# Kernel tuning notes

Hardware: AMD Instinct MI355X
Metric: run time of the kernel (lower is better)

## Reference

```python
import jax, jax.numpy as jnp
import numpy as np

DM, EXP, N, K, FRAC = 1024, 2, 16, 4, 16
D = DM * EXP            # working_dim = 2048
DTR = D // FRAC         # delta low-rank dim = 128
EPS = 1e-6


def setup_inputs() -> dict:
    key = jax.random.key(0)
    ks = jax.random.split(key, 12)
    s = lambda fan: 1.0 / np.sqrt(fan)
    x = jax.random.normal(ks[0], (2, 1024, DM), jnp.float32)
    rms_w = jnp.ones((DM,), jnp.float32)
    in_W = jax.random.normal(ks[1], (DM, 2 * D), jnp.float32) * s(DM)
    in_b = jax.random.normal(ks[2], (2 * D,), jnp.float32) * s(DM)
    conv_w = jax.random.normal(ks[3], (D, K), jnp.float32) * s(K)
    conv_b = jax.random.normal(ks[4], (D,), jnp.float32) * s(K)
    # A = arange(1..N) repeated over channels, stored as log
    A_log = jnp.log(jnp.tile(jnp.arange(1, N + 1, dtype=jnp.float32), (D, 1)))
    dbc_W = jax.random.normal(ks[5], (D, DTR + 2 * N), jnp.float32) * s(D)
    dbc_b = jax.random.normal(ks[6], (DTR + 2 * N,), jnp.float32) * s(D)
    dup_W = jax.random.normal(ks[7], (DTR, D), jnp.float32) * s(DTR)
    dup_b = jax.random.normal(ks[8], (D,), jnp.float32) * s(DTR)
    out_W = jax.random.normal(ks[9], (D, DM), jnp.float32) * s(D)
    out_b = jax.random.normal(ks[10], (DM,), jnp.float32) * s(D)
    return dict(x=x, rms_w=rms_w, in_W=in_W, in_b=in_b, conv_w=conv_w,
                conv_b=conv_b, A_log=A_log, dbc_W=dbc_W, dbc_b=dbc_b,
                dup_W=dup_W, dup_b=dup_b, out_W=out_W, out_b=out_b)


def _mamba_block(x, rms_w, in_W, in_b, conv_w, conv_b, A_log,
                 dbc_W, dbc_b, dup_W, dup_b, out_W, out_b):
    residual = x
    # RMSNorm
    h = x * jax.lax.rsqrt(jnp.mean(x * x, axis=-1, keepdims=True) + EPS) * rms_w
    # in projection -> (x1, g)
    proj = h @ in_W + in_b
    x1, g = proj[..., :D], proj[..., D:]
    # depthwise causal conv (torch pads K-1 both sides then keeps first T == left-pad K-1)
    xt = jnp.transpose(x1, (0, 2, 1))                      # [B, D, T]
    xc = jax.lax.conv_general_dilated(
        xt, conv_w[:, None, :], window_strides=(1,), padding=[(K - 1, 0)],
        feature_group_count=D, dimension_numbers=("NCH", "OIH", "NCH"))
    xc = xc + conv_b[:, None]
    x1 = jax.nn.silu(jnp.transpose(xc, (0, 2, 1)))         # [B, T, D]
    # selective SSM
    A = -jnp.exp(A_log)                                    # [D, N]
    dbc = x1 @ dbc_W + dbc_b
    delta, Bm, Cm = dbc[..., :DTR], dbc[..., DTR:DTR + N], dbc[..., DTR + N:]
    delta = jax.nn.softplus(delta @ dup_W + dup_b)         # [B, T, D]
    A_disc = jnp.exp(delta[..., None] * A)                 # [B, T, D, N]
    B_x = delta[..., None] * Bm[:, :, None, :] * x1[..., None]  # [B, T, D, N]
    # time-major sequential scan: h_t = A_t * h_{t-1} + Bx_t
    Ad_t = jnp.transpose(A_disc, (1, 0, 2, 3))
    Bx_t = jnp.transpose(B_x, (1, 0, 2, 3))

    def step(hc, inp):
        a, b = inp
        hc = a * hc + b
        return hc, hc

    h0 = jnp.zeros((x.shape[0], D, N), x1.dtype)
    _, hs = jax.lax.scan(step, h0, (Ad_t, Bx_t))           # [T, B, D, N]
    y = jnp.einsum("tbdn,btn->btd", hs, Cm)                # [B, T, D]
    # gate and out projection
    y = jax.nn.silu(g) * y
    out = y @ out_W + out_b
    return out + residual


def reference(x, rms_w, in_W, in_b, conv_w, conv_b, A_log,
              dbc_W, dbc_b, dup_W, dup_b, out_W, out_b):
    return _mamba_block(x, rms_w, in_W, in_b, conv_w, conv_b, A_log,
                        dbc_W, dbc_b, dup_W, dup_b, out_W, out_b)
```

## Files before the change

### kernel.cpp

```cpp
#include <hip/hip_runtime.h>
#include <math.h>

typedef unsigned short us;
typedef __attribute__((ext_vector_type(8))) short frag8;
typedef __attribute__((ext_vector_type(8))) unsigned short u8v;
typedef __attribute__((ext_vector_type(4))) float f4;
typedef __attribute__((ext_vector_type(2))) float f2;

#define B_   2
#define T_   1024
#define DM_  1024
#define D_   2048
#define N_   16
#define DTR_ 128
#define NDBC 160
#define ROWS (B_*T_)
#define EPS_ 1e-6f
#define NCH  32
#define CLEN (T_/NCH)
#define KSPL 8
#define OSPL 4
#define L2E  1.44269504f

__device__ __forceinline__ float us2f(us s){
    return __uint_as_float(((unsigned int)s) << 16);
}
__device__ __forceinline__ us f2us(float f){
    unsigned int u = __float_as_uint(f);
    return (us)((u + 0x7FFF + ((u >> 16) & 1)) >> 16);
}
__device__ __forceinline__ float exp2i(float x){
    float r; asm("v_exp_f32 %0, %1" : "=v"(r) : "v"(x)); return r;
}
__device__ __forceinline__ float rcpi(float x){
    return __builtin_amdgcn_rcpf(x);
}

__device__ __forceinline__ void async16(const void* g, void* l){
    __builtin_amdgcn_global_load_lds(
        (const __attribute__((address_space(1))) void*)g,
        (__attribute__((address_space(3)))       void*)l, 16, 0, 0);
}

template<int CTRL>
__device__ __forceinline__ float dpp_add(float x){
    int t = __builtin_amdgcn_update_dpp(0, __float_as_int(x), CTRL, 0xF, 0xF, true);
    return x + __int_as_float(t);
}
__device__ __forceinline__ float sum4_quad(float x){
    x = dpp_add<0xB1>(x);
    x = dpp_add<0x4E>(x);
    return x;
}

__global__ __launch_bounds__(256) void prep_weights(
    const float* __restrict__ in_W,  const float* __restrict__ out_W,
    const float* __restrict__ dbc_W, const float* __restrict__ dup_W,
    us* __restrict__ inWt, us* __restrict__ outWt,
    us* __restrict__ dbcWt, us* __restrict__ dupWt,
    const float* __restrict__ x, const float* __restrict__ rms_w,
    us* __restrict__ hbf)
{
    int bid = blockIdx.x;
    int tx = threadIdx.x, ty = threadIdx.y;
    if (bid >= 6720) {
        const int row = bid - 6720;
        const int tid = ty * 32 + tx;
        const float* xr = x + (size_t)row * DM_;
        float vals[4], ss = 0.f;
#pragma unroll
        for (int i = 0; i < 4; ++i) { vals[i] = xr[tid + i*256]; ss += vals[i]*vals[i]; }
#pragma unroll
        for (int off = 32; off >= 1; off >>= 1) ss += __shfl_xor(ss, off, 64);
        __shared__ float red[4];
        if ((tid & 63) == 0) red[tid >> 6] = ss;
        __syncthreads();
        float scale = rsqrtf((red[0]+red[1]+red[2]+red[3]) / (float)DM_ + EPS_);
#pragma unroll
        for (int i = 0; i < 4; ++i)
            hbf[(size_t)row * DM_ + tid + i*256] = f2us(vals[i] * scale * rms_w[tid + i*256]);
        return;
    }
    __shared__ us tile[32][33];
    const float* src; us* dst; int C, R, TX, rel;
    if (bid < 4096)      { src = in_W;  dst = inWt;  R = 1024; C = 4096; TX = 128; rel = bid; }
    else if (bid < 6144) { src = out_W; dst = outWt; R = 2048; C = 1024; TX = 32;  rel = bid - 4096; }
    else if (bid < 6464) { src = dbc_W; dst = dbcWt; R = 2048; C = 160;  TX = 5;   rel = bid - 6144; }
    else                 { src = dup_W; dst = dupWt; R = 128;  C = 2048; TX = 64;  rel = bid - 6464; }
    int c0 = (rel % TX) * 32, r0 = (rel / TX) * 32;
    for (int i = ty; i < 32; i += 8)
        tile[i][tx] = f2us(src[(size_t)(r0 + i) * C + c0 + tx]);
    __syncthreads();
    for (int i = ty; i < 32; i += 8)
        dst[(size_t)(c0 + i) * R + r0 + tx] = tile[tx][i];
}

__global__ __launch_bounds__(256) void transpose_us(const us* __restrict__ in,
                                                    us* __restrict__ out, int R, int C)
{
    __shared__ us tile[32][33];
    int c0 = blockIdx.x * 32, r0 = blockIdx.y * 32;
    int tx = threadIdx.x, ty = threadIdx.y;
    for (int i = ty; i < 32; i += 8)
        tile[i][tx] = in[(size_t)(r0 + i) * C + c0 + tx];
    __syncthreads();
    for (int i = ty; i < 32; i += 8)
        out[(size_t)(c0 + i) * R + r0 + tx] = tile[tx][i];
}

template<int EPI, bool RB>
__global__ __launch_bounds__(256) void mgemm(
    const us*    __restrict__ A,
    const us*    __restrict__ Bt,
    const float* __restrict__ bias,
    float*       __restrict__ Cf,
    us*          __restrict__ Caux,
    const float* __restrict__ resid,
    float*       __restrict__ bct,
    int M, int N, int K, int ld)
{
    __shared__ us As[128*64];
    __shared__ us Bs[128*64];
    const int tid = threadIdx.x;
    const int bm = blockIdx.y * 128;
    const int bn = blockIdx.x * 128;
    const int w = tid >> 6, lane = tid & 63;
    const int wr = w >> 1, wc = w & 1;
    const int m16 = lane & 15, quad = lane >> 4;

    const us* Ak = A;
    const us* Bk = Bt;
    if constexpr (EPI == 5) {
        const size_t koff = (size_t)blockIdx.z * K;
        Ak += koff; Bk += koff;
        Cf += (size_t)blockIdx.z * (size_t)M * N;
    }

    f4 acc[4][4];
#pragma unroll
    for (int i = 0; i < 4; ++i)
#pragma unroll
        for (int j = 0; j < 4; ++j)
            acc[i][j] = (f4){0.f, 0.f, 0.f, 0.f};

    for (int k0 = 0; k0 < K; k0 += 64) {
        __syncthreads();
#pragma unroll
        for (int q = 0; q < 4; ++q) {
            int cb = (w*4 + q)*64 + lane;
            int row = cb >> 3, c8 = (cb & 7)*8;
            async16(Ak + (size_t)(bm + row) * ld + k0 + c8, &As[cb*8]);
            async16(Bk + (size_t)(bn + row) * ld + k0 + c8, &Bs[cb*8]);
        }
        __syncthreads();
#pragma unroll
        for (int ks = 0; ks < 64; ks += 32) {
            frag8 af[4], bfr[4];
#pragma unroll
            for (int i = 0; i < 4; ++i)
                af[i] = *(const frag8*)&As[(wr*64 + i*16 + m16)*64 + ks + quad*8];
#pragma unroll
            for (int j = 0; j < 4; ++j)
                bfr[j] = *(const frag8*)&Bs[(wc*64 + j*16 + m16)*64 + ks + quad*8];
#pragma unroll
            for (int i = 0; i < 4; ++i)
#pragma unroll
                for (int j = 0; j < 4; ++j)
                    acc[i][j] = __builtin_amdgcn_mfma_f32_16x16x32_bf16(af[i], bfr[j], acc[i][j], 0, 0, 0);
        }
    }

#pragma unroll
    for (int i = 0; i < 4; ++i) {
#pragma unroll
        for (int j = 0; j < 4; ++j) {
            int col = bn + wc*64 + j*16 + m16;
            if (col >= N) continue;
            float bvc = (RB || EPI == 5) ? 0.f : bias[col];
#pragma unroll
            for (int r = 0; r < 4; ++r) {
                int row = bm + wr*64 + i*16 + quad*4 + r;
                float v = acc[i][j][r] + (EPI == 5 ? 0.f : (RB ? bias[row] : bvc));
                if constexpr (EPI == 1) {
                    v = fmaxf(v, 0.f) + __logf(1.f + __expf(-fabsf(v)));
                    Cf[(size_t)row * N + col] = v;
                } else if constexpr (EPI == 2) {
                    v += resid[(size_t)row * N + col];
                    Cf[(size_t)row * N + col] = v;
                } else if constexpr (EPI == 3) {
                    if (col < DTR_) Caux[(size_t)row * DTR_ + col] = f2us(v);
                    else            bct [(size_t)row * 32 + (col - DTR_)] = v;
                } else if constexpr (EPI == 4) {
                    if (col < D_) Cf  [(size_t)row * D_ + col]        = v;
                    else          Caux[(size_t)row * D_ + (col - D_)] = f2us(v);
                } else {
                    Cf[(size_t)row * N + col] = v;
                }
            }
        }
    }
}

__global__ __launch_bounds__(256) void dbc_reduce(
    const float* __restrict__ part,
    const float* __restrict__ bias,
    us*    __restrict__ dtrb,
    float* __restrict__ bct)
{
    int idx = blockIdx.x * 256 + threadIdx.x;
    int row = idx / NDBC, col = idx - row * NDBC;
    float v = bias[col];
#pragma unroll
    for (int z = 0; z < KSPL; ++z)
        v += part[(size_t)z * ROWS * NDBC + idx];
    if (col < DTR_) dtrb[(size_t)row * DTR_ + col] = f2us(v);
    else            bct [(size_t)row * 32 + (col - DTR_)] = v;
}

__global__ __launch_bounds__(256) void out_reduce(
    const float* __restrict__ part,
    const float* __restrict__ bias,
    const float* __restrict__ resid,
    float* __restrict__ out)
{
    int idx = (blockIdx.x * 256 + threadIdx.x) * 4;
    int col = idx & (DM_ - 1);
    f4 v = *(const f4*)&bias[col];
    v += *(const f4*)&resid[idx];
#pragma unroll
    for (int z = 0; z < OSPL; ++z)
        v += *(const f4*)&part[(size_t)z * ROWS * DM_ + idx];
    *(f4*)&out[idx] = v;
}

__global__ __launch_bounds__(256) void conv_silu_kernel(
    const float* __restrict__ x1pre,
    const us*    __restrict__ g_rm,
    const float* __restrict__ cw,
    const float* __restrict__ cb,
    us*          __restrict__ x1cb,
    us*          __restrict__ x1tb,
    us*          __restrict__ g_t)
{
    __shared__ us tileX[32][33];
    __shared__ us tileG[32][33];
    const int tx = threadIdx.x, ty = threadIdx.y;
    const int d0 = blockIdx.x * 32, r0 = blockIdx.y * 32;
    const int d = d0 + tx;
    const float w0 = cw[d*4+0], w1 = cw[d*4+1], w2 = cw[d*4+2], w3 = cw[d*4+3];
    const float bias = cb[d];
    for (int i = ty; i < 32; i += 8) {
        int row = r0 + i;
        int t = row & (T_ - 1);
        const float* base = x1pre + (size_t)row * D_ + d;
        float acc = bias;
        acc = fmaf(w3, base[0], acc);
        if (t >= 1) acc = fmaf(w2, base[-D_],   acc);
        if (t >= 2) acc = fmaf(w1, base[-2*D_], acc);
        if (t >= 3) acc = fmaf(w0, base[-3*D_], acc);
        float sg = rcpi(1.f + exp2i(-acc * L2E));
        us uv = f2us(acc * sg);
        x1cb[(size_t)row * D_ + d] = uv;
        tileX[i][tx] = uv;
        tileG[i][tx] = g_rm[(size_t)row * D_ + d];
    }
    __syncthreads();
    for (int i = ty; i < 32; i += 8) {
        x1tb[(size_t)(d0 + i) * ROWS + r0 + tx] = tileX[tx][i];
        g_t [(size_t)(d0 + i) * ROWS + r0 + tx] = tileG[tx][i];
    }
}

__global__ __launch_bounds__(128, 4) void scan_block_kernel(
    const float* __restrict__ delta_t,
    const us*    __restrict__ x1tb,
    const float* __restrict__ bct,
    const float* __restrict__ A_log,
    const us*    __restrict__ g_t,
    us*          __restrict__ y_t)
{
    __shared__ float ysA[T_ + NCH];
    __shared__ float ysB[T_ + NCH];
    __shared__ f4 PSl[2][NCH][9];

    const int tid = threadIdx.x;
    const int pr = blockIdx.x & (D_/2 - 1);
    const int b  = blockIdx.x >> 10;
    const int d0 = pr * 2;
    const int ng = tid & 3;
    const int c  = tid >> 2;
    const size_t rb  = (size_t)b * T_;
    const size_t cb0 = (size_t)d0 * ROWS + rb;
    const int t0 = c * CLEN;

    f4 al0 = *(const f4*)&A_log[d0 * N_ + ng * 4];
    f4 al1 = *(const f4*)&A_log[(d0 + 1) * N_ + ng * 4];
    const f2 aA01 = (f2){-__expf(al0[0])*L2E, -__expf(al0[1])*L2E};
    const f2 aA23 = (f2){-__expf(al0[2])*L2E, -__expf(al0[3])*L2E};
    const f2 aB01 = (f2){-__expf(al1[0])*L2E, -__expf(al1[1])*L2E};
    const f2 aB23 = (f2){-__expf(al1[2])*L2E, -__expf(al1[3])*L2E};

    const float* __restrict__ dpA = delta_t + cb0 + t0;
    const float* __restrict__ dpB = dpA + ROWS;
    const us*    __restrict__ xpA = x1tb + cb0 + t0;
    const us*    __restrict__ xpB = xpA + ROWS;
    const float* __restrict__ bp = bct + (size_t)(rb + t0) * 32 + ng * 4;
    const float* __restrict__ cp = bp + 16;

    float DsA = 0.f, DsB = 0.f;
    f2 SA01={0.f,0.f}, SA23={0.f,0.f};
    f2 SB01={0.f,0.f}, SB23={0.f,0.f};
#pragma unroll
    for (int g = 0; g < 4; ++g) {
        f4 dA0 = *(const f4*)&dpA[g*8], dA1 = *(const f4*)&dpA[g*8 + 4];
        f4 dB0 = *(const f4*)&dpB[g*8], dB1 = *(const f4*)&dpB[g*8 + 4];
        u8v xA = *(const u8v*)&xpA[g*8];
        u8v xB = *(const u8v*)&xpB[g*8];
#pragma unroll
        for (int j = 0; j < 8; ++j) {
            float djA = (j < 4) ? dA0[j] : dA1[j-4];
            float djB = (j < 4) ? dB0[j] : dB1[j-4];
            f4 Bv = *(const f4*)&bp[(size_t)(g*8 + j) * 32];
            float dxA = djA * us2f(xA[j]);
            float dxB = djB * us2f(xB[j]);
            DsA += djA; DsB += djB;
            f2 jA = (f2){djA, djA}, jB = (f2){djB, djB};
            f2 eA01 = jA*aA01, eA23 = jA*aA23;
            f2 eB01 = jB*aB01, eB23 = jB*aB23;
            f2 xA01 = (f2){exp2i(eA01.x), exp2i(eA01.y)};
            f2 xA23 = (f2){exp2i(eA23.x), exp2i(eA23.y)};
            f2 xB01 = (f2){exp2i(eB01.x), exp2i(eB01.y)};
            f2 xB23 = (f2){exp2i(eB23.x), exp2i(eB23.y)};
            SA01 = xA01*SA01 + (f2){dxA*Bv[0], dxA*Bv[1]};
            SA23 = xA23*SA23 + (f2){dxA*Bv[2], dxA*Bv[3]};
            SB01 = xB01*SB01 + (f2){dxB*Bv[0], dxB*Bv[1]};
            SB23 = xB23*SB23 + (f2){dxB*Bv[2], dxB*Bv[3]};
        }
    }
    f2 PA01 = (f2){exp2i(aA01.x*DsA), exp2i(aA01.y*DsA)};
    f2 PA23 = (f2){exp2i(aA23.x*DsA), exp2i(aA23.y*DsA)};
    f2 PB01 = (f2){exp2i(aB01.x*DsB), exp2i(aB01.y*DsB)};
    f2 PB23 = (f2){exp2i(aB23.x*DsB), exp2i(aB23.y*DsB)};
    PSl[0][c][2*ng+0] = (f4){PA01.x,PA01.y,SA01.x,SA01.y};
    PSl[0][c][2*ng+1] = (f4){PA23.x,PA23.y,SA23.x,SA23.y};
    PSl[1][c][2*ng+0] = (f4){PB01.x,PB01.y,SB01.x,SB01.y};
    PSl[1][c][2*ng+1] = (f4){PB23.x,PB23.y,SB23.x,SB23.y};
    __syncthreads();

    f2 hA01={0.f,0.f}, hA23={0.f,0.f}, hB01={0.f,0.f}, hB23={0.f,0.f};
    for (int c2 = 0; c2 < c; ++c2) {
        f4 p0 = PSl[0][c2][2*ng+0], p1 = PSl[0][c2][2*ng+1];
        f4 q0 = PSl[1][c2][2*ng+0], q1 = PSl[1][c2][2*ng+1];
        hA01 = (f2){p0[0],p0[1]}*hA01 + (f2){p0[2],p0[3]};
        hA23 = (f2){p1[0],p1[1]}*hA23 + (f2){p1[2],p1[3]};
        hB01 = (f2){q0[0],q0[1]}*hB01 + (f2){q0[2],q0[3]};
        hB23 = (f2){q1[0],q1[1]}*hB23 + (f2){q1[2],q1[3]};
    }

#pragma unroll
    for (int g = 0; g < 4; ++g) {
        f4 dA0 = *(const f4*)&dpA[g*8], dA1 = *(const f4*)&dpA[g*8 + 4];
        f4 dB0 = *(const f4*)&dpB[g*8], dB1 = *(const f4*)&dpB[g*8 + 4];
        u8v xA = *(const u8v*)&xpA[g*8];
        u8v xB = *(const u8v*)&xpB[g*8];
#pragma unroll
        for (int j = 0; j < 8; ++j) {
            float djA = (j < 4) ? dA0[j] : dA1[j-4];
            float djB = (j < 4) ? dB0[j] : dB1[j-4];
            f4 Bv = *(const f4*)&bp[(size_t)(g*8 + j) * 32];
            f4 Cv = *(const f4*)&cp[(size_t)(g*8 + j) * 32];
            float dxA = djA * us2f(xA[j]);
            float dxB = djB * us2f(xB[j]);
            f2 jA = (f2){djA, djA}, jB = (f2){djB, djB};
            f2 eA01 = jA*aA01, eA23 = jA*aA23;
            f2 eB01 = jB*aB01, eB23 = jB*aB23;
            f2 xA01 = (f2){exp2i(eA01.x), exp2i(eA01.y)};
            f2 xA23 = (f2){exp2i(eA23.x), exp2i(eA23.y)};
            f2 xB01 = (f2){exp2i(eB01.x), exp2i(eB01.y)};
            f2 xB23 = (f2){exp2i(eB23.x), exp2i(eB23.y)};
            hA01 = xA01*hA01 + (f2){dxA*Bv[0], dxA*Bv[1]};
            hA23 = xA23*hA23 + (f2){dxA*Bv[2], dxA*Bv[3]};
            hB01 = xB01*hB01 + (f2){dxB*Bv[0], dxB*Bv[1]};
            hB23 = xB23*hB23 + (f2){dxB*Bv[2], dxB*Bv[3]};
            float sA = (hA01.x*Cv[0] + hA01.y*Cv[1]) + (hA23.x*Cv[2] + hA23.y*Cv[3]);
            float sB = (hB01.x*Cv[0] + hB01.y*Cv[1]) + (hB23.x*Cv[2] + hB23.y*Cv[3]);
            sA = sum4_quad(sA);
            sB = sum4_quad(sB);
            int t = t0 + g*8 + j;
            if (ng == 0) { ysA[t + (t >> 5)] = sA; ysB[t + (t >> 5)] = sB; }
        }
    }
    __syncthreads();

    {
        int i = tid * 8;
        int fi = i + (i >> 5);
        u8v ugA = *(const u8v*)&g_t[cb0 + i];
        u8v ugB = *(const u8v*)&g_t[cb0 + ROWS + i];
        u8v uyA, uyB;
#pragma unroll
        for (int k = 0; k < 8; ++k) {
            float gA = us2f(ugA[k]), gB = us2f(ugB[k]);
            uyA[k] = f2us(ysA[fi + k] * gA * rcpi(1.f + exp2i(-gA * L2E)));
            uyB[k] = f2us(ysB[fi + k] * gB * rcpi(1.f + exp2i(-gB * L2E)));
        }
        *(u8v*)&y_t[cb0 + i] = uyA;
        *(u8v*)&y_t[cb0 + ROWS + i] = uyB;
    }
}

extern "C" void kernel_launch(void* const* d_in, const int* in_sizes, int n_in,
                              void* d_out, int out_size, void* d_ws, size_t ws_size,
                              hipStream_t stream)
{
    const float* x      = (const float*)d_in[0];
    const float* rms_w  = (const float*)d_in[1];
    const float* in_W   = (const float*)d_in[2];
    const float* in_b   = (const float*)d_in[3];
    const float* conv_w = (const float*)d_in[4];
    const float* conv_b = (const float*)d_in[5];
    const float* A_log  = (const float*)d_in[6];
    const float* dbc_W  = (const float*)d_in[7];
    const float* dbc_b  = (const float*)d_in[8];
    const float* dup_W  = (const float*)d_in[9];
    const float* dup_b  = (const float*)d_in[10];
    const float* out_W  = (const float*)d_in[11];
    const float* out_b  = (const float*)d_in[12];
    float* out = (float*)d_out;

    float* ws      = (float*)d_ws;
    float* x1pre   = ws;
    us* g_rm  = (us*)(x1pre + (size_t)ROWS*D_);
    us* g_t   = g_rm  + (size_t)ROWS*D_;
    float* bct     = (float*)(g_t + (size_t)ROWS*D_);
    float* delta_t = bct + (size_t)2*N_*ROWS;
    us* hbf   = (us*)(delta_t + (size_t)ROWS*D_);
    us* x1cb  = hbf   + (size_t)ROWS*DM_;
    us* x1tb  = x1cb  + (size_t)ROWS*D_;
    us* dtrb  = x1tb  + (size_t)ROWS*D_;
    us* inWt  = dtrb  + (size_t)ROWS*DTR_;
    us* dbcWt = inWt  + (size_t)2*D_*DM_;
    us* dupWt = dbcWt + (size_t)NDBC*D_;
    us* outWt = dupWt + (size_t)D_*DTR_;
    float* dbcPart = x1pre;
    us* y_t   = (us*)x1pre;
    us* ybf   = x1cb;
    float* outPart = x1pre;
    dim3 tb(32, 8);
    prep_weights<<<6720 + ROWS, tb, 0, stream>>>(in_W, out_W, dbc_W, dup_W,
                                                 inWt, outWt, dbcWt, dupWt,
                                                 x, rms_w, hbf);
    mgemm<4,false><<<dim3(32, 16), 256, 0, stream>>>(
        hbf, inWt, in_b, x1pre, g_rm, nullptr, nullptr, ROWS, 2*D_, DM_, DM_);
    conv_silu_kernel<<<dim3(D_/32, ROWS/32), tb, 0, stream>>>(
        x1pre, g_rm, conv_w, conv_b, x1cb, x1tb, g_t);
    mgemm<5,false><<<dim3(2, 16, KSPL), 256, 0, stream>>>(
        x1cb, dbcWt, nullptr, dbcPart, nullptr, nullptr, nullptr,
        ROWS, NDBC, D_/KSPL, D_);
    dbc_reduce<<<ROWS*NDBC/256, 256, 0, stream>>>(dbcPart, dbc_b, dtrb, bct);
    mgemm<1,true><<<dim3(16, 16), 256, 0, stream>>>(
        dupWt, dtrb, dup_b, delta_t, nullptr, nullptr, nullptr, D_, ROWS, DTR_, DTR_);
    scan_block_kernel<<<B_*D_/2, 128, 0, stream>>>(delta_t, x1tb, bct, A_log, g_t, y_t);
    transpose_us<<<dim3(ROWS/32, D_/32), tb, 0, stream>>>(y_t, ybf, D_, ROWS);
    mgemm<5,false><<<dim3(8, 16, OSPL), 256, 0, stream>>>(
        ybf, outWt, nullptr, outPart, nullptr, nullptr, nullptr,
        ROWS, DM_, D_/OSPL, D_);
    out_reduce<<<ROWS*DM_/1024, 256, 0, stream>>>(outPart, out_b, x, out);
}
```

Baseline: 244.2 us.

## Fuse y transpose into scan epilogue and swizzle GEMM block order

The scan kernel now writes the gated output straight into the row-major bf16 buffer used by the out projection, packing the two channels as one 32-bit store per timestep. This removes the separate transpose kernel and its round trip through memory. The GEMM kernels also remap block indices with an 8-way swizzle, intended to improve L2 reuse across blocks that run at the same time. The fused stores are strided 4-byte writes (stride D_), so they are poorly coalesced. The swizzle assumes the grid size is divisible by 8.

```diff
diff --git a/kernel.cpp b/kernel.cpp
--- a/kernel.cpp
+++ b/kernel.cpp
@@ -95,19 +95,6 @@
         dst[(size_t)(c0 + i) * R + r0 + tx] = tile[tx][i];
 }
 
-__global__ __launch_bounds__(256) void transpose_us(const us* __restrict__ in,
-                                                    us* __restrict__ out, int R, int C)
-{
-    __shared__ us tile[32][33];
-    int c0 = blockIdx.x * 32, r0 = blockIdx.y * 32;
-    int tx = threadIdx.x, ty = threadIdx.y;
-    for (int i = ty; i < 32; i += 8)
-        tile[i][tx] = in[(size_t)(r0 + i) * C + c0 + tx];
-    __syncthreads();
-    for (int i = ty; i < 32; i += 8)
-        out[(size_t)(c0 + i) * R + r0 + tx] = tile[tx][i];
-}
-
 template<int EPI, bool RB>
 __global__ __launch_bounds__(256) void mgemm(
     const us*    __restrict__ A,
@@ -122,8 +109,12 @@
     __shared__ us As[128*64];
     __shared__ us Bs[128*64];
     const int tid = threadIdx.x;
-    const int bm = blockIdx.y * 128;
-    const int bn = blockIdx.x * 128;
+    const int nx  = gridDim.x;
+    const int lin = blockIdx.y * nx + blockIdx.x;
+    const int cpx = (nx * gridDim.y) >> 3;
+    const int swz = (lin & 7) * cpx + (lin >> 3);
+    const int bm = (swz / nx) * 128;
+    const int bn = (swz % nx) * 128;
     const int w = tid >> 6, lane = tid & 63;
     const int wr = w >> 1, wc = w & 1;
     const int m16 = lane & 15, quad = lane >> 4;
@@ -277,7 +268,7 @@
     const float* __restrict__ bct,
     const float* __restrict__ A_log,
     const us*    __restrict__ g_t,
-    us*          __restrict__ y_t)
+    us*          __restrict__ ybf)
 {
     __shared__ float ysA[T_ + NCH];
     __shared__ float ysB[T_ + NCH];
@@ -397,15 +388,14 @@
         int fi = i + (i >> 5);
         u8v ugA = *(const u8v*)&g_t[cb0 + i];
         u8v ugB = *(const u8v*)&g_t[cb0 + ROWS + i];
-        u8v uyA, uyB;
 #pragma unroll
         for (int k = 0; k < 8; ++k) {
             float gA = us2f(ugA[k]), gB = us2f(ugB[k]);
-            uyA[k] = f2us(ysA[fi + k] * gA * rcpi(1.f + exp2i(-gA * L2E)));
-            uyB[k] = f2us(ysB[fi + k] * gB * rcpi(1.f + exp2i(-gB * L2E)));
-        }
-        *(u8v*)&y_t[cb0 + i] = uyA;
-        *(u8v*)&y_t[cb0 + ROWS + i] = uyB;
+            float yA = ysA[fi + k] * gA * rcpi(1.f + exp2i(-gA * L2E));
+            float yB = ysB[fi + k] * gB * rcpi(1.f + exp2i(-gB * L2E));
+            unsigned int pk = (unsigned int)f2us(yA) | ((unsigned int)f2us(yB) << 16);
+            *(unsigned int*)&ybf[(size_t)(rb + i + k) * D_ + d0] = pk;
+        }
     }
 }
 
@@ -443,7 +433,6 @@
     us* dupWt = dbcWt + (size_t)NDBC*D_;
     us* outWt = dupWt + (size_t)D_*DTR_;
     float* dbcPart = x1pre;
-    us* y_t   = (us*)x1pre;
     us* ybf   = x1cb;
     float* outPart = x1pre;
     dim3 tb(32, 8);
@@ -460,8 +449,7 @@
     dbc_reduce<<<ROWS*NDBC/256, 256, 0, stream>>>(dbcPart, dbc_b, dtrb, bct);
     mgemm<1,true><<<dim3(16, 16), 256, 0, stream>>>(
         dupWt, dtrb, dup_b, delta_t, nullptr, nullptr, nullptr, D_, ROWS, DTR_, DTR_);
-    scan_block_kernel<<<B_*D_/2, 128, 0, stream>>>(delta_t, x1tb, bct, A_log, g_t, y_t);
-    transpose_us<<<dim3(ROWS/32, D_/32), tb, 0, stream>>>(y_t, ybf, D_, ROWS);
+    scan_block_kernel<<<B_*D_/2, 128, 0, stream>>>(delta_t, x1tb, bct, A_log, g_t, ybf);
     mgemm<5,false><<<dim3(8, 16, OSPL), 256, 0, stream>>>(
         ybf, outWt, nullptr, outPart, nullptr, nullptr, nullptr,
         ROWS, DM_, D_/OSPL, D_);
```

Result: slower. 253.2 us (+3.7%).
